# Optimization experiments

Hardware: AMD Instinct MI355X
Metric: run time of the kernel (lower is better)

Reference implementation:

```python
import jax, jax.numpy as jnp
from jax import lax
import numpy as np

# StyleLayer config (see init_kwargs)
B, CIN, COUT, SDIM, K, H, W = 8, 512, 512, 512, 3, 64, 64
UP, DOWN = 2, 2
PAD = (9, 8, 9, 8)            # px0, px1, py0, py1 (computed in __init__)
GAIN = 2.0 ** 0.5             # non-rgb gain
SLOPE = 0.2                   # non-rgb negative slope
CLAMP = 256.0                 # conv_clamp
TAPS = 12                     # filter_size * factor
TMP_SRATE = 128.0             # max(sr_in, sr_out) * lrelu_sampling
CUTOFF = 32.0
WIDTH = 32.0                  # half_width * 2


def _kaiser_lowpass(numtaps, cutoff, width, fs):
    """Equivalent of scipy.signal.firwin(numtaps, cutoff, width=width, fs=fs)."""
    nyq = fs / 2.0
    atten = 2.285 * (numtaps - 1) * np.pi * (width / nyq) + 7.95  # kaiser_atten
    if atten > 50:
        beta = 0.1102 * (atten - 8.7)
    elif atten > 21:
        beta = 0.5842 * (atten - 21) ** 0.4 + 0.07886 * (atten - 21)
    else:
        beta = 0.0
    m = np.arange(numtaps) - (numtaps - 1) / 2.0
    fc = cutoff / nyq
    h = fc * np.sinc(fc * m) * np.kaiser(numtaps, beta)
    h /= h.sum()
    return jnp.asarray(h, jnp.float32)


def _upfirdn2d_sep(x, f, up, down, padding, gain):
    """upfirdn2d reference with separable 1D filter (flip_filter=False)."""
    Bx, C, Hx, Wx = x.shape
    px0, px1, py0, py1 = padding
    if up > 1:  # zero insertion
        x = x.reshape(Bx, C, Hx, 1, Wx, 1)
        x = jnp.pad(x, [(0, 0), (0, 0), (0, 0), (0, up - 1), (0, 0), (0, up - 1)])
        x = x.reshape(Bx, C, Hx * up, Wx * up)
    x = jnp.pad(x, [(0, 0), (0, 0), (py0, py1), (px0, px1)])
    fk = (f * (gain ** 0.5))[::-1].astype(x.dtype)  # gain**(ndim/2) per pass, flipped
    t = fk.shape[0]
    dn = ('NCHW', 'OIHW', 'NCHW')
    kx = jnp.tile(fk.reshape(1, 1, 1, t), (C, 1, 1, 1))
    x = lax.conv_general_dilated(x, kx, (1, 1), [(0, 0), (0, 0)], dimension_numbers=dn, feature_group_count=C)
    ky = jnp.tile(fk.reshape(1, 1, t, 1), (C, 1, 1, 1))
    x = lax.conv_general_dilated(x, ky, (1, 1), [(0, 0), (0, 0)], dimension_numbers=dn, feature_group_count=C)
    if down > 1:
        x = x[:, :, ::down, ::down]
    return x


def setup_inputs() -> dict:
    key = jax.random.key(0)
    ks = jax.random.split(key, 4)
    f = _kaiser_lowpass(TAPS, CUTOFF, WIDTH, TMP_SRATE)
    return {
        'x': jax.random.normal(ks[0], (B, CIN, H, W), jnp.float32),
        'w': jax.random.normal(ks[1], (B, SDIM), jnp.float32),
        'affine_weight': jax.random.normal(ks[2], (CIN, SDIM), jnp.float32),
        'affine_bias': jnp.ones((CIN,), jnp.float32),  # bias.data.fill_(1.0)
        'conv_weight': jax.random.normal(ks[3], (COUT, CIN, K, K), jnp.float32),
        'bias': jnp.zeros((COUT,), jnp.float32),
        'up_filter': f,
        'down_filter': f,
        'ema': jnp.ones((1,), jnp.float32),
    }


def reference(x, w, affine_weight, affine_bias, conv_weight, bias, up_filter, down_filter, ema):
    input_gain = lax.rsqrt(ema[0])
    # affine: Linear with scale = 1/sqrt(style_dim), linear activation
    s = w @ (affine_weight * (1.0 / SDIM ** 0.5)).T + affine_bias            # [B, CIN]
    # modulated conv weight construction
    wt = conv_weight[None] * s[:, None, :, None, None] * (1.0 / (CIN * K * K) ** 0.5)
    d = lax.rsqrt(jnp.sum(jnp.square(wt), axis=(2, 3, 4)) + 1e-8)            # demod
    wt = wt * d[:, :, None, None, None] * input_gain
    # grouped conv: one group per sample, padding = kernel_size - 1
    xg = x.reshape(1, B * CIN, H, W)
    wg = wt.reshape(B * COUT, CIN, K, K)
    y = lax.conv_general_dilated(xg, wg, (1, 1), [(K - 1, K - 1), (K - 1, K - 1)],
                                 dimension_numbers=('NCHW', 'OIHW', 'NCHW'),
                                 feature_group_count=B)
    y = y.reshape(B, COUT, H + K - 1, W + K - 1)
    # filtered_lrelu reference: bias -> up-FIR (gain=up^2) -> lrelu*gain, clamp -> FIR-down
    y = y + bias[None, :, None, None]
    y = _upfirdn2d_sep(y, up_filter, UP, 1, PAD, float(UP * UP))
    y = jnp.clip(jnp.where(y >= 0, y, y * SLOPE) * GAIN, -CLAMP, CLAMP)
    y = _upfirdn2d_sep(y, down_filter, 1, DOWN, (0, 0, 0, 0), 1.0)
    return y
```

## Files before the change

### kernel.cpp

```cpp
#include <hip/hip_runtime.h>
#include <hip/hip_bf16.h>


#define B_    8
#define CIN_  512
#define COUT_ 512
#define SDIM_ 512
#define H_    64
#define W_    64
#define HO_   66
#define NPIX  4356
#define XP    68

typedef short s8v  __attribute__((ext_vector_type(8)));
typedef float f4v  __attribute__((ext_vector_type(4)));

#define WAITV3() asm volatile("s_waitcnt vmcnt(3)" ::: "memory")
#define WAITV0() asm volatile("s_waitcnt vmcnt(0)" ::: "memory")

__global__ void k_style_s(const float* __restrict__ w, const float* __restrict__ aw,
                          const float* __restrict__ ab, float* __restrict__ s) {
    int t = blockIdx.x * blockDim.x + threadIdx.x;
    int b = t >> 9, c = t & 511;
    const float inv = 0.044194173824159216f;
    const float* wp = w + b * SDIM_;
    const float* ap = aw + c * SDIM_;
    float acc = 0.f;
    for (int k = 0; k < SDIM_; ++k) acc += wp[k] * ap[k];
    s[t] = acc * inv + ab[c];
}

__global__ void k_style_r(const float* __restrict__ cw, float* __restrict__ r) {
    int t = blockIdx.x * blockDim.x + threadIdx.x;
    const float* p = cw + t * 9;
    float a = 0.f;
    #pragma unroll
    for (int k = 0; k < 9; ++k) a += p[k] * p[k];
    r[t] = a;
}

__global__ void k_style_coef(const float* __restrict__ s, const float* __restrict__ r,
                             const float* __restrict__ ema, float* __restrict__ coef) {
    int t = blockIdx.x * blockDim.x + threadIdx.x;
    int b = t >> 9, o = t & 511;
    const float scale2 = 1.0f / 4608.0f;
    const float* sp = s + b * 512;
    const float* rp = r + o * 512;
    float acc = 0.f;
    for (int c = 0; c < 512; ++c) { float sv = sp[c]; acc += sv * sv * rp[c]; }
    float d  = rsqrtf(scale2 * acc + 1e-8f);
    float ig = rsqrtf(ema[0]);
    coef[t] = d * ig * 0.014731391274719739f;
}

__global__ __launch_bounds__(256) void k_prep_w(const float* __restrict__ cw,
                                                __hip_bfloat16* __restrict__ wb) {
    int t = blockIdx.x * 256 + threadIdx.x;
    int tap = t / (512 * 512);
    int rem = t - tap * 512 * 512;
    int o = rem >> 9, c = rem & 511;
    wb[t] = __float2bfloat16(cw[(o * 512 + c) * 9 + tap]);
}

__global__ __launch_bounds__(256) void k_prep_x(const float* __restrict__ x,
                                                const float* __restrict__ s,
                                                __hip_bfloat16* __restrict__ xt) {
    __shared__ float tile[64][65];
    const int y = blockIdx.x;
    const int b = blockIdx.y;
    const int tid = threadIdx.x;
    const bool yin = (y >= 2 && y < 66);
    __hip_bfloat16* orow = xt + ((size_t)(b * XP + y)) * XP * 512;
    for (int c0 = 0; c0 < 512; c0 += 64) {
        if (yin) {
            for (int i = tid; i < 64 * 64; i += 256) {
                int c = i >> 6, xx = i & 63;
                tile[c][xx] = x[(((size_t)b * 512 + c0 + c) * 64 + (y - 2)) * 64 + xx]
                              * s[b * 512 + c0 + c];
            }
        }
        __syncthreads();
        for (int j = tid; j < 68 * 8; j += 256) {
            int xx = j >> 3, cg = j & 7;
            bool xin = yin && (xx >= 2 && xx < 66);
            union { ushort u[8]; float4 f4; } pk;
            #pragma unroll
            for (int k = 0; k < 8; ++k) {
                float v = xin ? tile[cg * 8 + k][xx - 2] : 0.f;
                __hip_bfloat16 h = __float2bfloat16(v);
                pk.u[k] = *reinterpret_cast<ushort*>(&h);
            }
            *reinterpret_cast<float4*>(orow + (size_t)xx * 512 + c0 + cg * 8) = pk.f4;
        }
        __syncthreads();
    }
}

__device__ __forceinline__ void gload16u(const char* base, unsigned voff, void* l) {
    __builtin_amdgcn_global_load_lds(
        (const __attribute__((address_space(1))) unsigned*)(base + voff),
        (__attribute__((address_space(3))) unsigned*)l, 16, 0, 0);
}

__global__ __launch_bounds__(512) void k_conv_mfma(
    const __hip_bfloat16* __restrict__ wb, const __hip_bfloat16* __restrict__ xt,
    const float* __restrict__ coef, const float* __restrict__ bias,
    __hip_bfloat16* __restrict__ y1)
{
    __shared__ __hip_bfloat16 lds[3][12288];

    int flat = blockIdx.x + 35 * (blockIdx.y + 2 * blockIdx.z);
    { int xcd = flat & 7, idx = flat >> 3; flat = xcd * 70 + idx; }
    const int pi = flat % 35;
    const int t2 = flat / 35;
    const int b  = t2 & 7;
    const int o0 = (t2 >> 3) * 256;
    const int p0 = pi * 128;

    const int tid = threadIdx.x, wv = tid >> 6, ln = tid & 63;
    const int wm = wv >> 1, wn = wv & 1;

    const char* wbB = (const char*)wb;
    const char* xtB = (const char*)(xt + (size_t)b * XP * XP * 512);
    const int srow = tid >> 2, ssl = tid & 3;
    const unsigned swzs = (unsigned)((ssl ^ ((srow >> 1) & 3)) << 3);
    unsigned voffA0 = ((unsigned)(o0 + srow) * 512u + swzs) * 2u;
    unsigned voffA1 = ((unsigned)(o0 + 128 + srow) * 512u + swzs) * 2u;
    unsigned voffB0;
    {
        int p = p0 + srow; if (p > NPIX - 1) p = NPIX - 1;
        int py = (int)(((unsigned)p * 63551u) >> 22);
        int px = p - py * 66;
        voffB0 = ((unsigned)(py * XP + px) * 512u + swzs) * 2u;
    }

    int aoff[4], boff[4];
    #pragma unroll
    for (int f = 0; f < 4; ++f) {
        int r  = wm * 64 + f * 16 + (ln & 15);
        aoff[f] = (r * 32 + (((ln >> 4) ^ ((r >> 1) & 3)) << 3)) * 2;
        int rb = wn * 64 + f * 16 + (ln & 15);
        boff[f] = (8192 + rb * 32 + (((ln >> 4) ^ ((rb >> 1) & 3)) << 3)) * 2;
    }

    f4v acc[4][4];
    #pragma unroll
    for (int fm = 0; fm < 4; ++fm)
        #pragma unroll
        for (int fn = 0; fn < 4; ++fn) acc[fm][fn] = (f4v){0.f, 0.f, 0.f, 0.f};

    auto stage = [&](int st, int buf) {
        int tap = st >> 4;
        int ki  = (tap * 11) >> 5;
        int kj  = tap - ki * 3;
        unsigned ccb  = (unsigned)(st & 15) << 6;
        unsigned offA = (unsigned)tap * 524288u + ccb;
        unsigned offB = (unsigned)(ki * XP + kj) * 1024u + ccb;
        __hip_bfloat16* dst = &lds[buf][0] + wv * 512;
        gload16u(wbB, voffA0 + offA, dst);
        gload16u(wbB, voffA1 + offA, dst + 4096);
        gload16u(xtB, voffB0 + offB, dst + 8192);
    };

    auto compute = [&](int buf) {
        const char* base = (const char*)&lds[buf][0];
        s8v af[4], bfv[4];
        #pragma unroll
        for (int f = 0; f < 4; ++f) {
            af[f]  = *reinterpret_cast<const s8v*>(base + aoff[f]);
            bfv[f] = *reinterpret_cast<const s8v*>(base + boff[f]);
        }
        #pragma unroll
        for (int fm = 0; fm < 4; ++fm)
            #pragma unroll
            for (int fn = 0; fn < 4; ++fn)
                acc[fm][fn] = __builtin_amdgcn_mfma_f32_16x16x32_bf16(
                    af[fm], bfv[fn], acc[fm][fn], 0, 0, 0);
    };

    stage(0, 0);
    stage(1, 1);

    #pragma unroll 1
    for (int st = 0; st < 141; st += 3) {
        WAITV3(); __builtin_amdgcn_s_barrier();
        compute(0); stage(st + 2, 2);
        WAITV3(); __builtin_amdgcn_s_barrier();
        compute(1); stage(st + 3, 0);
        WAITV3(); __builtin_amdgcn_s_barrier();
        compute(2); stage(st + 4, 1);
    }
    WAITV3(); __builtin_amdgcn_s_barrier();
    compute(0); stage(143, 2);
    WAITV3(); __builtin_amdgcn_s_barrier();
    compute(1);
    WAITV0(); __builtin_amdgcn_s_barrier();
    compute(2);

    #pragma unroll
    for (int fm = 0; fm < 4; ++fm) {
        #pragma unroll
        for (int fn = 0; fn < 4; ++fn) {
            int p = p0 + wn * 64 + fn * 16 + (ln & 15);
            if (p < NPIX) {
                int ob = o0 + wm * 64 + fm * 16 + (ln >> 4) * 4;
                #pragma unroll
                for (int j = 0; j < 4; ++j) {
                    int o = ob + j;
                    float v = acc[fm][fn][j] * coef[b * 512 + o] + bias[o];
                    y1[((size_t)(b * 512 + o)) * NPIX + p] = __float2bfloat16(v);
                }
            }
        }
    }
}

__global__ __launch_bounds__(256) void k_style_fir(
    const __hip_bfloat16* __restrict__ y1, const float* __restrict__ uf,
    const float* __restrict__ df, float* __restrict__ out)
{
    __shared__ float smA[5632];
    __shared__ float smB[3200];
    float* It = smA;
    float* hu = smB;
    float* zt = smA;
    float* dh = smB;

    const int img = blockIdx.z;
    const int oy0 = blockIdx.y * 32;
    const int ox0 = blockIdx.x * 32;
    const int tid = threadIdx.x;
    const __hip_bfloat16* I = y1 + (size_t)img * NPIX;

    float cu[12], cd[12];
    #pragma unroll
    for (int q = 0; q < 12; ++q) { cu[q] = uf[q]; cd[q] = df[q]; }

    const int ty = tid >> 5, tx = tid & 31;
    const int ty4 = tid >> 4, tx4 = tid & 15;

    #pragma unroll
    for (int k = 0; k < 6; ++k) {
        int rr = ty + 8 * k; if (rr >= 42) break;
        int gy = oy0 - 4 + rr;
        bool yin = (gy >= 0 && gy < HO_);
        #pragma unroll
        for (int j = 0; j < 2; ++j) {
            int cc = tx + 32 * j; if (cc >= 42) continue;
            int gx = ox0 - 4 + cc;
            float v = 0.f;
            if (yin && gx >= 0 && gx < HO_) v = __bfloat162float(I[gy * HO_ + gx]);
            It[rr * 44 + cc] = v;
        }
    }
    __syncthreads();

    #pragma unroll
    for (int k = 0; k < 6; ++k) {
        int m = ty + 8 * k; if (m >= 42) break;
        #pragma unroll
        for (int j = 0; j < 2; ++j) {
            int h = tx + 32 * j; if (h >= 37) continue;
            float v[6];
            #pragma unroll
            for (int q = 0; q < 6; ++q) v[q] = It[m * 44 + h + 5 - q];
            float e = 0.f, o = 0.f;
            #pragma unroll
            for (int q = 0; q < 6; ++q) { e += cu[2 * q] * v[q]; o += cu[2 * q + 1] * v[q]; }
            *reinterpret_cast<float2*>(hu + m * 76 + 2 * h) = make_float2(2.f * e, 2.f * o);
        }
    }
    __syncthreads();

    #pragma unroll
    for (int k = 0; k < 5; ++k) {
        int r = ty + 8 * k; if (r >= 37) break;
        #pragma unroll
        for (int j = 0; j < 3; ++j) {
            int rx = tx + 32 * j; if (rx >= 74) continue;
            float v[6];
            #pragma unroll
            for (int q = 0; q < 6; ++q) v[q] = hu[(r + 5 - q) * 76 + rx];
            float e = 0.f, o = 0.f;
            #pragma unroll
            for (int q = 0; q < 6; ++q) { e += cu[2 * q] * v[q]; o += cu[2 * q + 1] * v[q]; }
            e *= 2.f; o *= 2.f;
            e = (e >= 0.f ? e : e * 0.2f) * 1.4142135623730951f;
            o = (o >= 0.f ? o : o * 0.2f) * 1.4142135623730951f;
            e = fminf(fmaxf(e, -256.f), 256.f);
            o = fminf(fmaxf(o, -256.f), 256.f);
            zt[(2 * r) * 76 + rx] = e;
            zt[(2 * r + 1) * 76 + rx] = o;
        }
    }
    __syncthreads();

    #pragma unroll
    for (int k = 0; k < 5; ++k) {
        int ry = ty4 + 16 * k; if (ry >= 74) break;
        const float* zr = zt + ry * 76 + 4 * tx4;
        float z[14];
        #pragma unroll
        for (int t = 0; t < 7; ++t) {
            float2 p2 = *reinterpret_cast<const float2*>(zr + 2 * t);
            z[2 * t] = p2.x; z[2 * t + 1] = p2.y;
        }
        float a0 = 0.f, a1 = 0.f;
        #pragma unroll
        for (int u = 0; u < 12; ++u) { a0 += z[u] * cd[11 - u]; a1 += z[u + 2] * cd[11 - u]; }
        *reinterpret_cast<float2*>(dh + ry * 36 + 2 * tx4) = make_float2(a0, a1);
    }
    __syncthreads();

    #pragma unroll
    for (int k = 0; k < 2; ++k) {
        int r2 = ty + 8 * k;
        float d[14];
        #pragma unroll
        for (int v = 0; v < 14; ++v) d[v] = dh[(4 * r2 + v) * 36 + tx];
        float a0 = 0.f, a1 = 0.f;
        #pragma unroll
        for (int v = 0; v < 12; ++v) { a0 += d[v] * cd[11 - v]; a1 += d[v + 2] * cd[11 - v]; }
        float* op = out + (size_t)img * 64 * 64 + (oy0 + 2 * r2) * 64 + ox0 + tx;
        op[0]  = a0;
        op[64] = a1;
    }
}

extern "C" void kernel_launch(void* const* d_in, const int* in_sizes, int n_in,
                              void* d_out, int out_size, void* d_ws, size_t ws_size,
                              hipStream_t stream) {
    const float* x    = (const float*)d_in[0];
    const float* w    = (const float*)d_in[1];
    const float* aw   = (const float*)d_in[2];
    const float* ab   = (const float*)d_in[3];
    const float* cw   = (const float*)d_in[4];
    const float* bias = (const float*)d_in[5];
    const float* uf   = (const float*)d_in[6];
    const float* df   = (const float*)d_in[7];
    const float* ema  = (const float*)d_in[8];
    float* out = (float*)d_out;

    float* ws   = (float*)d_ws;
    float* s_   = ws;
    float* coef = ws + 4096;
    float* r_   = ws + 8192;
    __hip_bfloat16* y1 = (__hip_bfloat16*)(ws + 270336);
    __hip_bfloat16* xt = (__hip_bfloat16*)(ws + 270336 + 8921088);
    __hip_bfloat16* wb = (__hip_bfloat16*)(ws + 270336 + 8921088 + 9469952);

    k_style_s   <<<16,   256, 0, stream>>>(w, aw, ab, s_);
    k_style_r   <<<1024, 256, 0, stream>>>(cw, r_);
    k_style_coef<<<16,   256, 0, stream>>>(s_, r_, ema, coef);
    k_prep_w    <<<9216, 256, 0, stream>>>(cw, wb);
    k_prep_x    <<<dim3(68, 8), 256, 0, stream>>>(x, s_, xt);
    k_conv_mfma <<<dim3(35, 2, 8), 512, 0, stream>>>(wb, xt, coef, bias, y1);
    k_style_fir <<<dim3(2, 2, 4096), 256, 0, stream>>>(y1, uf, df, out);
}
```

Baseline: 417.3 us.

## Halve conv block to 4 waves with larger per-wave MFMA tile

The MFMA conv kernel now runs 256 threads (4 waves) per block instead of 512, and each wave computes a 128x64 output tile (8x4 MFMA fragments) instead of 64x64. Each thread issues six global-to-LDS loads per stage instead of three, and the wait count is raised to match. The goal is more MFMA work per LDS fragment read and fewer waves syncing at each barrier, with launch bounds asking for two blocks per CU. The cost is doubled accumulator registers, which may limit occupancy or cause spills, and fewer waves available to hide latency.

Measured after the change: 422.7 us. About the same (+1.3%).

```diff
diff --git a/kernel.cpp b/kernel.cpp
--- a/kernel.cpp
+++ b/kernel.cpp
@@ -15,7 +15,7 @@
 typedef short s8v  __attribute__((ext_vector_type(8)));
 typedef float f4v  __attribute__((ext_vector_type(4)));
 
-#define WAITV3() asm volatile("s_waitcnt vmcnt(3)" ::: "memory")
+#define WAITV6() asm volatile("s_waitcnt vmcnt(6)" ::: "memory")
 #define WAITV0() asm volatile("s_waitcnt vmcnt(0)" ::: "memory")
 
 __global__ void k_style_s(const float* __restrict__ w, const float* __restrict__ aw,
@@ -102,7 +102,7 @@
         (__attribute__((address_space(3))) unsigned*)l, 16, 0, 0);
 }
 
-__global__ __launch_bounds__(512) void k_conv_mfma(
+__global__ __launch_bounds__(256, 2) void k_conv_mfma(
     const __hip_bfloat16* __restrict__ wb, const __hip_bfloat16* __restrict__ xt,
     const float* __restrict__ coef, const float* __restrict__ bias,
     __hip_bfloat16* __restrict__ y1)
@@ -122,30 +122,40 @@
 
     const char* wbB = (const char*)wb;
     const char* xtB = (const char*)(xt + (size_t)b * XP * XP * 512);
-    const int srow = tid >> 2, ssl = tid & 3;
-    const unsigned swzs = (unsigned)((ssl ^ ((srow >> 1) & 3)) << 3);
-    unsigned voffA0 = ((unsigned)(o0 + srow) * 512u + swzs) * 2u;
-    unsigned voffA1 = ((unsigned)(o0 + 128 + srow) * 512u + swzs) * 2u;
-    unsigned voffB0;
-    {
-        int p = p0 + srow; if (p > NPIX - 1) p = NPIX - 1;
+    unsigned voffA[4], voffB[2];
+    #pragma unroll
+    for (int i = 0; i < 4; ++i) {
+        int j = i * 256 + tid;
+        int row = j >> 2, sl = j & 3;
+        unsigned swz = (unsigned)((sl ^ ((row >> 1) & 3)) << 3);
+        voffA[i] = ((unsigned)(o0 + row) * 512u + swz) * 2u;
+    }
+    #pragma unroll
+    for (int i = 0; i < 2; ++i) {
+        int j = i * 256 + tid;
+        int row = j >> 2, sl = j & 3;
+        unsigned swz = (unsigned)((sl ^ ((row >> 1) & 3)) << 3);
+        int p = p0 + row; if (p > NPIX - 1) p = NPIX - 1;
         int py = (int)(((unsigned)p * 63551u) >> 22);
         int px = p - py * 66;
-        voffB0 = ((unsigned)(py * XP + px) * 512u + swzs) * 2u;
-    }
-
-    int aoff[4], boff[4];
+        voffB[i] = ((unsigned)(py * XP + px) * 512u + swz) * 2u;
+    }
+
+    int aoff[8], boff[4];
+    #pragma unroll
+    for (int f = 0; f < 8; ++f) {
+        int r  = wm * 128 + f * 16 + (ln & 15);
+        aoff[f] = (r * 32 + (((ln >> 4) ^ ((r >> 1) & 3)) << 3)) * 2;
+    }
     #pragma unroll
     for (int f = 0; f < 4; ++f) {
-        int r  = wm * 64 + f * 16 + (ln & 15);
-        aoff[f] = (r * 32 + (((ln >> 4) ^ ((r >> 1) & 3)) << 3)) * 2;
         int rb = wn * 64 + f * 16 + (ln & 15);
         boff[f] = (8192 + rb * 32 + (((ln >> 4) ^ ((rb >> 1) & 3)) << 3)) * 2;
     }
 
-    f4v acc[4][4];
-    #pragma unroll
-    for (int fm = 0; fm < 4; ++fm)
+    f4v acc[8][4];
+    #pragma unroll
+    for (int fm = 0; fm < 8; ++fm)
         #pragma unroll
         for (int fn = 0; fn < 4; ++fn) acc[fm][fn] = (f4v){0.f, 0.f, 0.f, 0.f};
 
@@ -157,21 +167,25 @@
         unsigned offA = (unsigned)tap * 524288u + ccb;
         unsigned offB = (unsigned)(ki * XP + kj) * 1024u + ccb;
         __hip_bfloat16* dst = &lds[buf][0] + wv * 512;
-        gload16u(wbB, voffA0 + offA, dst);
-        gload16u(wbB, voffA1 + offA, dst + 4096);
-        gload16u(xtB, voffB0 + offB, dst + 8192);
+        #pragma unroll
+        for (int i = 0; i < 4; ++i)
+            gload16u(wbB, voffA[i] + offA, dst + i * 2048);
+        #pragma unroll
+        for (int i = 0; i < 2; ++i)
+            gload16u(xtB, voffB[i] + offB, dst + 8192 + i * 2048);
     };
 
     auto compute = [&](int buf) {
         const char* base = (const char*)&lds[buf][0];
-        s8v af[4], bfv[4];
-        #pragma unroll
-        for (int f = 0; f < 4; ++f) {
+        s8v af[8], bfv[4];
+        #pragma unroll
+        for (int f = 0; f < 8; ++f)
             af[f]  = *reinterpret_cast<const s8v*>(base + aoff[f]);
+        #pragma unroll
+        for (int f = 0; f < 4; ++f)
             bfv[f] = *reinterpret_cast<const s8v*>(base + boff[f]);
-        }
-        #pragma unroll
-        for (int fm = 0; fm < 4; ++fm)
+        #pragma unroll
+        for (int fm = 0; fm < 8; ++fm)
             #pragma unroll
             for (int fn = 0; fn < 4; ++fn)
                 acc[fm][fn] = __builtin_amdgcn_mfma_f32_16x16x32_bf16(
@@ -183,27 +197,27 @@
 
     #pragma unroll 1
     for (int st = 0; st < 141; st += 3) {
-        WAITV3(); __builtin_amdgcn_s_barrier();
+        WAITV6(); __builtin_amdgcn_s_barrier();
         compute(0); stage(st + 2, 2);
-        WAITV3(); __builtin_amdgcn_s_barrier();
+        WAITV6(); __builtin_amdgcn_s_barrier();
         compute(1); stage(st + 3, 0);
-        WAITV3(); __builtin_amdgcn_s_barrier();
+        WAITV6(); __builtin_amdgcn_s_barrier();
         compute(2); stage(st + 4, 1);
     }
-    WAITV3(); __builtin_amdgcn_s_barrier();
+    WAITV6(); __builtin_amdgcn_s_barrier();
     compute(0); stage(143, 2);
-    WAITV3(); __builtin_amdgcn_s_barrier();
+    WAITV6(); __builtin_amdgcn_s_barrier();
     compute(1);
     WAITV0(); __builtin_amdgcn_s_barrier();
     compute(2);
 
     #pragma unroll
-    for (int fm = 0; fm < 4; ++fm) {
+    for (int fm = 0; fm < 8; ++fm) {
         #pragma unroll
         for (int fn = 0; fn < 4; ++fn) {
             int p = p0 + wn * 64 + fn * 16 + (ln & 15);
             if (p < NPIX) {
-                int ob = o0 + wm * 64 + fm * 16 + (ln >> 4) * 4;
+                int ob = o0 + wm * 128 + fm * 16 + (ln >> 4) * 4;
                 #pragma unroll
                 for (int j = 0; j < 4; ++j) {
                     int o = ob + j;
@@ -354,6 +368,6 @@
     k_style_coef<<<16,   256, 0, stream>>>(s_, r_, ema, coef);
     k_prep_w    <<<9216, 256, 0, stream>>>(cw, wb);
     k_prep_x    <<<dim3(68, 8), 256, 0, stream>>>(x, s_, xt);
-    k_conv_mfma <<<dim3(35, 2, 8), 512, 0, stream>>>(wb, xt, coef, bias, y1);
+    k_conv_mfma <<<dim3(35, 2, 8), 256, 0, stream>>>(wb, xt, coef, bias, y1);
     k_style_fir <<<dim3(2, 2, 4096), 256, 0, stream>>>(y1, uf, df, out);
 }
```
